# Kernel tuning notes

Hardware: AMD Instinct MI355X
Metric: run time of the kernel (lower is better)

## Reference

```python
import jax, jax.numpy as jnp
import numpy as np

B, SQ, SD, H = 64, 64, 512, 128


def setup_inputs() -> dict:
    key = jax.random.key(0)
    k1, k2, k3, k4, k5 = jax.random.split(key, 5)
    q = jax.random.normal(k1, (B, SQ, H), dtype=jnp.float32)
    d_pos = jax.random.normal(k2, (B, SD, H), dtype=jnp.float32)
    d_neg = jax.random.normal(k3, (B, SD, H), dtype=jnp.float32)
    mask_pos = jax.random.randint(k4, (B, SD), 0, 2, dtype=jnp.int32).at[:, 0].set(1)
    mask_neg = jax.random.randint(k5, (B, SD), 0, 2, dtype=jnp.int32).at[:, 0].set(1)
    return {"q": q, "d_pos": d_pos, "d_neg": d_neg,
            "mask_pos": mask_pos, "mask_neg": mask_neg}


def _colbert_maxsim(q, d, mask):
    # q: [a, s, h], d: [b, t, h], mask: [b, t] -> scores [a, b]
    simis = jnp.einsum('ash,bth->abst', q, d)            # [a, b, s, t]
    simis = jnp.where(mask[None, :, None, :] == 0, -jnp.inf, simis)
    return simis.max(axis=3).sum(axis=2)                 # max over t, sum over s


def reference(q, d_pos, d_neg, mask_pos, mask_neg):
    # Concatenate pos and in-batch-negative score blocks -> [B, 2B]
    distances = jnp.concatenate(
        [_colbert_maxsim(q, d_pos, mask_pos),
         _colbert_maxsim(q, d_neg, mask_neg)], axis=1)
    labels = jnp.arange(q.shape[0])
    logp = jax.nn.log_softmax(distances, axis=1)
    loss = -jnp.take_along_axis(logp, labels[:, None], axis=1).mean()
    return loss
```

## Files before the change

kernel.cpp:

```cpp
#include <hip/hip_runtime.h>
#include <hip/hip_bf16.h>
#include <math.h>
#include <stdint.h>

#define BB 64
#define SQN 64
#define SDN 512
#define HH 128

typedef __attribute__((ext_vector_type(8))) short bf16x8;
typedef __attribute__((ext_vector_type(16))) float f32x16;

__device__ __forceinline__ short f2bf(float f) {
  union { float f; unsigned u; } x; x.f = f;
  unsigned r = x.u + 0x7fffu + ((x.u >> 16) & 1u);
  return (short)(r >> 16);
}

__device__ __forceinline__ void gl_lds16(const short* g, short* l) {
  __builtin_amdgcn_global_load_lds(
      (const __attribute__((address_space(1))) unsigned int*)g,
      (__attribute__((address_space(3))) unsigned int*)l, 16, 0, 0);
}

__global__ __launch_bounds__(256)
void convert_all(const float* __restrict__ q, const float* __restrict__ dp,
                 const float* __restrict__ dn,
                 const int* __restrict__ mp, const int* __restrict__ mn,
                 short* __restrict__ oq, short* __restrict__ od,
                 int* __restrict__ nchunks, int* __restrict__ nvalid,
                 int* __restrict__ counter) {
  const int D_BLOCKS = (2 * BB * SDN) / 8;
  if (blockIdx.x < D_BLOCKS) {
    const int bs = blockIdx.x >> 6;
    const int j0 = (blockIdx.x & 63) * 8;
    const int side = bs >> 6, b = bs & 63;
    const int* mask = (side ? mn : mp) + b * SDN;

    __shared__ int s_perm[8];
    __shared__ int s_pad32;

    if (threadIdx.x < 64) {
      const int ln = threadIdx.x;
      int mreg[8];
      #pragma unroll
      for (int it = 0; it < 8; ++it) mreg[it] = mask[it * 64 + ln];
      int run = 0;
      #pragma unroll
      for (int it = 0; it < 8; ++it) {
        unsigned long long bal = __ballot(mreg[it] != 0);
        int pos = run + __popcll(bal & ((1ull << ln) - 1ull));
        if (mreg[it]) {
          unsigned rel = (unsigned)(pos - j0);
          if (rel < 8u) s_perm[rel] = it * 64 + ln;
        }
        run += (int)__popcll(bal);
      }
      if (ln < 8 && j0 + ln >= run) s_perm[ln] = -1;
      if (ln == 0) {
        s_pad32 = (run + 31) & ~31;
        if (j0 == 0) {
          nchunks[bs] = ((run + 127) & ~127) >> 7;
          nvalid[bs]  = run;
        }
      }
    }
    __syncthreads();

    const int j = j0 + (threadIdx.x >> 5);
    if (j >= s_pad32) return;
    const int l32 = threadIdx.x & 31;
    const int src_t = s_perm[threadIdx.x >> 5];
    const float* srcmat = side ? dn : dp;
    float4 v = make_float4(0.f, 0.f, 0.f, 0.f);
    if (src_t >= 0)
      v = ((const float4*)(srcmat + ((size_t)b * SDN + src_t) * HH))[l32];
    short4 o; o.x = f2bf(v.x); o.y = f2bf(v.y); o.z = f2bf(v.z); o.w = f2bf(v.w);
    *(short4*)&od[((size_t)bs * SDN + j) * HH + l32 * 4] = o;
  } else {
    if (blockIdx.x == D_BLOCKS && threadIdx.x == 0) *counter = 0;
    int i = (blockIdx.x - D_BLOCKS) * 256 + threadIdx.x;
    float4 v = ((const float4*)q)[i];
    short4 o; o.x = f2bf(v.x); o.y = f2bf(v.y); o.z = f2bf(v.z); o.w = f2bf(v.w);
    *(short4*)&oq[i * 4] = o;
  }
}

#define ITS_OF(bi_, tc_) \
  (((tc_) == nchv[bi_] - 1) ? (((nvv[bi_] - ((tc_) << 7) + 31) >> 5) << 1) : 8)

__global__ __launch_bounds__(256, 2)
void maxsim_kernel(const short* __restrict__ qb,
                   const short* __restrict__ dc,
                   const int* __restrict__ nchunks,
                   const int* __restrict__ nvalid,
                   float* __restrict__ scores,
                   int* __restrict__ counter,
                   float* __restrict__ out) {
  const int lid  = blockIdx.x + 16 * blockIdx.y;
  const int xcd  = lid & 7;
  const int slot = lid >> 3;
  const int aslc = slot & 15;
  const int bs0  = (xcd + 8 * (slot >> 4)) * 4;

  __shared__ __align__(16) short d_lds[2][128 * 128];

  const int tid = threadIdx.x;
  const int ln  = tid & 63;
  const int w   = tid >> 6;
  const int l31 = ln & 31;
  const int kh  = ln >> 5;
  const int a   = aslc * 4 + w;

  int nchv[4], nvv[4];
  #pragma unroll
  for (int i = 0; i < 4; ++i) {
    nchv[i] = nchunks[bs0 + i];
    nvv[i]  = nvalid[bs0 + i];
  }

  bf16x8 qfrag[2][8];
  #pragma unroll
  for (int half = 0; half < 2; ++half) {
    const short* qrow = qb + ((size_t)a * SQN + half * 32 + l31) * HH + kh * 8;
    #pragma unroll
    for (int kc = 0; kc < 8; ++kc)
      qfrag[half][kc] = *(const bf16x8*)(qrow + kc * 16);
  }

  float rmaxh[2] = {0.f, 0.f};

  int cur_its = ITS_OF(0, 0);

  {
    const short* dsrc = dc + (size_t)bs0 * SDN * HH;
    #pragma unroll
    for (int it = 0; it < 8; ++it) {
      if (it < cur_its) {
        int f = it * 256 + tid;
        int row = f >> 4;
        int c = (f & 15) ^ (row & 15);
        gl_lds16(&dsrc[row * HH + c * 8], &d_lds[0][(it * 256 + w * 64) * 8]);
      }
    }
  }
  __syncthreads();

  int bi = 0, tc = 0, buf = 0;
  for (;;) {
    int nbi = bi, ntc = tc + 1;
    if (ntc == nchv[bi]) { ntc = 0; nbi = bi + 1; }
    const bool hn = (nbi < 4);
    const int nxt_its = hn ? ITS_OF(nbi, ntc) : 0;

    if (hn) {
      const short* dsrc = dc + ((size_t)(bs0 + nbi) * SDN + ntc * 128) * HH;
      short* dst = &d_lds[buf ^ 1][0];
      #pragma unroll
      for (int it = 0; it < 8; ++it) {
        if (it < nxt_its) {
          int f = it * 256 + tid;
          int row = f >> 4;
          int c = (f & 15) ^ (row & 15);
          gl_lds16(&dsrc[row * HH + c * 8], &dst[(it * 256 + w * 64) * 8]);
        }
      }
    }

    const int ntt = cur_its >> 1;
    const short* bufp = &d_lds[buf][0];
    #pragma unroll
    for (int tt = 0; tt < 4; ++tt) {
      if (tt < ntt) {
        int trow = tt * 32 + l31;
        int tm = trow & 15;
        const short* bbase = &bufp[trow * HH];
        f32x16 acc0 = {0,0,0,0,0,0,0,0,0,0,0,0,0,0,0,0};
        f32x16 acc1 = {0,0,0,0,0,0,0,0,0,0,0,0,0,0,0,0};
        #pragma unroll
        for (int kc = 0; kc < 8; ++kc) {
          int c = (kc * 2 + kh) ^ tm;
          bf16x8 dfrag = *(const bf16x8*)&bbase[c * 8];
          acc0 = __builtin_amdgcn_mfma_f32_32x32x16_bf16(dfrag, qfrag[0][kc], acc0, 0, 0, 0);
          acc1 = __builtin_amdgcn_mfma_f32_32x32x16_bf16(dfrag, qfrag[1][kc], acc1, 0, 0, 0);
        }
        float m0 = acc0[0], m1 = acc1[0];
        #pragma unroll
        for (int r = 1; r < 16; ++r) {
          m0 = fmaxf(m0, acc0[r]);
          m1 = fmaxf(m1, acc1[r]);
        }
        rmaxh[0] = fmaxf(rmaxh[0], m0);
        rmaxh[1] = fmaxf(rmaxh[1], m1);
      }
    }

    if (ntc == 0) {
      float v0 = fmaxf(rmaxh[0], __shfl_xor(rmaxh[0], 32));
      float v1 = fmaxf(rmaxh[1], __shfl_xor(rmaxh[1], 32));
      float s = v0 + v1;
      s += __shfl_xor(s, 1);  s += __shfl_xor(s, 2);  s += __shfl_xor(s, 4);
      s += __shfl_xor(s, 8);  s += __shfl_xor(s, 16);
      if (ln == 0)
        __hip_atomic_store(&scores[(size_t)a * (2 * BB) + bs0 + bi], s,
                           __ATOMIC_RELAXED, __HIP_MEMORY_SCOPE_AGENT);
      rmaxh[0] = 0.f; rmaxh[1] = 0.f;
    }

    __syncthreads();
    if (!hn) break;
    bi = nbi; tc = ntc; buf ^= 1; cur_its = nxt_its;
  }

  asm volatile("s_waitcnt vmcnt(0)" ::: "memory");
  __shared__ int s_ticket;
  if (tid == 0)
    s_ticket = __hip_atomic_fetch_add(counter, 1,
                                      __ATOMIC_RELAXED, __HIP_MEMORY_SCOPE_AGENT);
  __syncthreads();
  if (s_ticket != 511) return;

  __shared__ float part[16];
  #pragma unroll
  for (int q8 = 0; q8 < 4; ++q8) {
    int vp = w * 4 + q8;
    float acc = 0.f;
    #pragma unroll
    for (int i = 0; i < 4; ++i) {
      int r = vp * 4 + i;
      float v0 = __hip_atomic_load(&scores[r * 128 + ln],
                                   __ATOMIC_RELAXED, __HIP_MEMORY_SCOPE_AGENT);
      float v1 = __hip_atomic_load(&scores[r * 128 + 64 + ln],
                                   __ATOMIC_RELAXED, __HIP_MEMORY_SCOPE_AGENT);
      float mx = fmaxf(v0, v1);
      #pragma unroll
      for (int off = 32; off >= 1; off >>= 1) mx = fmaxf(mx, __shfl_xor(mx, off));
      float e = __expf(v0 - mx) + __expf(v1 - mx);
      #pragma unroll
      for (int off = 32; off >= 1; off >>= 1) e += __shfl_xor(e, off);
      float lse = mx + __logf(e);
      float diag = __shfl(v0, r);
      acc += lse - diag;
    }
    if (ln == 0) part[vp] = acc;
  }
  __syncthreads();
  if (w == 0) {
    float v = (ln < 16) ? part[ln] : 0.f;
    #pragma unroll
    for (int off = 8; off >= 1; off >>= 1) v += __shfl_xor(v, off);
    if (ln == 0) out[0] = v * (1.0f / 64.0f);
  }
}

extern "C" void kernel_launch(void* const* d_in, const int* in_sizes, int n_in,
                              void* d_out, int out_size, void* d_ws, size_t ws_size,
                              hipStream_t stream) {
  const float* q        = (const float*)d_in[0];
  const float* d_pos    = (const float*)d_in[1];
  const float* d_neg    = (const float*)d_in[2];
  const int*   mask_pos = (const int*)d_in[3];
  const int*   mask_neg = (const int*)d_in[4];

  short* q_bf = (short*)d_ws;
  short* d_c  = q_bf + (size_t)BB * SQN * HH;
  int*   nchunks = (int*)(d_c + (size_t)2 * BB * SDN * HH);
  int*   nvalid  = nchunks + 128;
  float* scores  = (float*)(nvalid + 128);
  int*   counter = (int*)(scores + 64 * 128);

  const int D_BLOCKS = (2 * BB * SDN) / 8;
  const int Q_BLOCKS = (BB * SQN * HH / 4) / 256;
  convert_all<<<D_BLOCKS + Q_BLOCKS, 256, 0, stream>>>(
      q, d_pos, d_neg, mask_pos, mask_neg, q_bf, d_c, nchunks, nvalid, counter);

  dim3 grid(16 , 32 );
  maxsim_kernel<<<grid, 256, 0, stream>>>(q_bf, d_c, nchunks, nvalid, scores,
                                          counter, (float*)d_out);
}
```

Baseline: 126.8 us.

## Split query halves across two waves with 512-thread blocks

Blocks grow from 256 to 512 threads, with two waves per query row: each handles one 32-row half of the query tokens, holding one accumulator instead of two. The half-sums are combined through shared memory with an extra block barrier at each document boundary. D tile loads are spread over twice as many threads. The aim is more waves in flight and lower register pressure per wave, at the cost of extra barriers and possibly fewer resident blocks given the 64KB LDS per block.

```diff
diff --git a/kernel.cpp b/kernel.cpp
--- a/kernel.cpp
+++ b/kernel.cpp
@@ -87,9 +87,9 @@
 }
 
 #define ITS_OF(bi_, tc_) \
-  (((tc_) == nchv[bi_] - 1) ? (((nvv[bi_] - ((tc_) << 7) + 31) >> 5) << 1) : 8)
-
-__global__ __launch_bounds__(256, 2)
+  (((tc_) == nchv[bi_] - 1) ? ((nvv[bi_] - ((tc_) << 7) + 31) >> 5) : 4)
+
+__global__ __launch_bounds__(512, 4)
 void maxsim_kernel(const short* __restrict__ qb,
                    const short* __restrict__ dc,
                    const int* __restrict__ nchunks,
@@ -104,13 +104,18 @@
   const int bs0  = (xcd + 8 * (slot >> 4)) * 4;
 
   __shared__ __align__(16) short d_lds[2][128 * 128];
-
-  const int tid = threadIdx.x;
-  const int ln  = tid & 63;
-  const int w   = tid >> 6;
-  const int l31 = ln & 31;
-  const int kh  = ln >> 5;
-  const int a   = aslc * 4 + w;
+  __shared__ float s_fin[4 * 32];
+  __shared__ int s_ticket;
+  __shared__ float part[16];
+
+  const int tid  = threadIdx.x;
+  const int ln   = tid & 63;
+  const int w    = tid >> 6;
+  const int l31  = ln & 31;
+  const int kh   = ln >> 5;
+  const int aw   = w >> 1;
+  const int half = w & 1;
+  const int a    = aslc * 4 + aw;
 
   int nchv[4], nvv[4];
   #pragma unroll
@@ -119,28 +124,27 @@
     nvv[i]  = nvalid[bs0 + i];
   }
 
-  bf16x8 qfrag[2][8];
-  #pragma unroll
-  for (int half = 0; half < 2; ++half) {
+  bf16x8 qfrag[8];
+  {
     const short* qrow = qb + ((size_t)a * SQN + half * 32 + l31) * HH + kh * 8;
     #pragma unroll
     for (int kc = 0; kc < 8; ++kc)
-      qfrag[half][kc] = *(const bf16x8*)(qrow + kc * 16);
-  }
-
-  float rmaxh[2] = {0.f, 0.f};
+      qfrag[kc] = *(const bf16x8*)(qrow + kc * 16);
+  }
+
+  float rmax = 0.f;
 
   int cur_its = ITS_OF(0, 0);
 
   {
     const short* dsrc = dc + (size_t)bs0 * SDN * HH;
     #pragma unroll
-    for (int it = 0; it < 8; ++it) {
+    for (int it = 0; it < 4; ++it) {
       if (it < cur_its) {
-        int f = it * 256 + tid;
+        int f = it * 512 + tid;
         int row = f >> 4;
         int c = (f & 15) ^ (row & 15);
-        gl_lds16(&dsrc[row * HH + c * 8], &d_lds[0][(it * 256 + w * 64) * 8]);
+        gl_lds16(&dsrc[row * HH + c * 8], &d_lds[0][(it * 512 + w * 64) * 8]);
       }
     }
   }
@@ -157,17 +161,17 @@
       const short* dsrc = dc + ((size_t)(bs0 + nbi) * SDN + ntc * 128) * HH;
       short* dst = &d_lds[buf ^ 1][0];
       #pragma unroll
-      for (int it = 0; it < 8; ++it) {
+      for (int it = 0; it < 4; ++it) {
         if (it < nxt_its) {
-          int f = it * 256 + tid;
+          int f = it * 512 + tid;
           int row = f >> 4;
           int c = (f & 15) ^ (row & 15);
-          gl_lds16(&dsrc[row * HH + c * 8], &dst[(it * 256 + w * 64) * 8]);
-        }
-      }
-    }
-
-    const int ntt = cur_its >> 1;
+          gl_lds16(&dsrc[row * HH + c * 8], &dst[(it * 512 + w * 64) * 8]);
+        }
+      }
+    }
+
+    const int ntt = cur_its;
     const short* bufp = &d_lds[buf][0];
     #pragma unroll
     for (int tt = 0; tt < 4; ++tt) {
@@ -175,36 +179,33 @@
         int trow = tt * 32 + l31;
         int tm = trow & 15;
         const short* bbase = &bufp[trow * HH];
-        f32x16 acc0 = {0,0,0,0,0,0,0,0,0,0,0,0,0,0,0,0};
-        f32x16 acc1 = {0,0,0,0,0,0,0,0,0,0,0,0,0,0,0,0};
+        f32x16 acc = {0,0,0,0,0,0,0,0,0,0,0,0,0,0,0,0};
         #pragma unroll
         for (int kc = 0; kc < 8; ++kc) {
           int c = (kc * 2 + kh) ^ tm;
           bf16x8 dfrag = *(const bf16x8*)&bbase[c * 8];
-          acc0 = __builtin_amdgcn_mfma_f32_32x32x16_bf16(dfrag, qfrag[0][kc], acc0, 0, 0, 0);
-          acc1 = __builtin_amdgcn_mfma_f32_32x32x16_bf16(dfrag, qfrag[1][kc], acc1, 0, 0, 0);
-        }
-        float m0 = acc0[0], m1 = acc1[0];
-        #pragma unroll
-        for (int r = 1; r < 16; ++r) {
-          m0 = fmaxf(m0, acc0[r]);
-          m1 = fmaxf(m1, acc1[r]);
-        }
-        rmaxh[0] = fmaxf(rmaxh[0], m0);
-        rmaxh[1] = fmaxf(rmaxh[1], m1);
+          acc = __builtin_amdgcn_mfma_f32_32x32x16_bf16(dfrag, qfrag[kc], acc, 0, 0, 0);
+        }
+        float m0 = acc[0];
+        #pragma unroll
+        for (int r = 1; r < 16; ++r) m0 = fmaxf(m0, acc[r]);
+        rmax = fmaxf(rmax, m0);
       }
     }
 
     if (ntc == 0) {
-      float v0 = fmaxf(rmaxh[0], __shfl_xor(rmaxh[0], 32));
-      float v1 = fmaxf(rmaxh[1], __shfl_xor(rmaxh[1], 32));
-      float s = v0 + v1;
-      s += __shfl_xor(s, 1);  s += __shfl_xor(s, 2);  s += __shfl_xor(s, 4);
-      s += __shfl_xor(s, 8);  s += __shfl_xor(s, 16);
-      if (ln == 0)
-        __hip_atomic_store(&scores[(size_t)a * (2 * BB) + bs0 + bi], s,
-                           __ATOMIC_RELAXED, __HIP_MEMORY_SCOPE_AGENT);
-      rmaxh[0] = 0.f; rmaxh[1] = 0.f;
+      float v = fmaxf(rmax, __shfl_xor(rmax, 32));
+      if (half && kh == 0) s_fin[aw * 32 + l31] = v;
+      __syncthreads();
+      if (!half) {
+        float s = v + s_fin[aw * 32 + l31];
+        s += __shfl_xor(s, 1);  s += __shfl_xor(s, 2);  s += __shfl_xor(s, 4);
+        s += __shfl_xor(s, 8);  s += __shfl_xor(s, 16);
+        if (ln == 0)
+          __hip_atomic_store(&scores[(size_t)a * (2 * BB) + bs0 + bi], s,
+                             __ATOMIC_RELAXED, __HIP_MEMORY_SCOPE_AGENT);
+      }
+      rmax = 0.f;
     }
 
     __syncthreads();
@@ -213,36 +214,36 @@
   }
 
   asm volatile("s_waitcnt vmcnt(0)" ::: "memory");
-  __shared__ int s_ticket;
   if (tid == 0)
     s_ticket = __hip_atomic_fetch_add(counter, 1,
                                       __ATOMIC_RELAXED, __HIP_MEMORY_SCOPE_AGENT);
   __syncthreads();
   if (s_ticket != 511) return;
 
-  __shared__ float part[16];
-  #pragma unroll
-  for (int q8 = 0; q8 < 4; ++q8) {
-    int vp = w * 4 + q8;
-    float acc = 0.f;
-    #pragma unroll
-    for (int i = 0; i < 4; ++i) {
-      int r = vp * 4 + i;
-      float v0 = __hip_atomic_load(&scores[r * 128 + ln],
-                                   __ATOMIC_RELAXED, __HIP_MEMORY_SCOPE_AGENT);
-      float v1 = __hip_atomic_load(&scores[r * 128 + 64 + ln],
-                                   __ATOMIC_RELAXED, __HIP_MEMORY_SCOPE_AGENT);
-      float mx = fmaxf(v0, v1);
-      #pragma unroll
-      for (int off = 32; off >= 1; off >>= 1) mx = fmaxf(mx, __shfl_xor(mx, off));
-      float e = __expf(v0 - mx) + __expf(v1 - mx);
-      #pragma unroll
-      for (int off = 32; off >= 1; off >>= 1) e += __shfl_xor(e, off);
-      float lse = mx + __logf(e);
-      float diag = __shfl(v0, r);
-      acc += lse - diag;
-    }
-    if (ln == 0) part[vp] = acc;
+  if (w < 4) {
+    #pragma unroll
+    for (int q8 = 0; q8 < 4; ++q8) {
+      int vp = w * 4 + q8;
+      float acc = 0.f;
+      #pragma unroll
+      for (int i = 0; i < 4; ++i) {
+        int r = vp * 4 + i;
+        float v0 = __hip_atomic_load(&scores[r * 128 + ln],
+                                     __ATOMIC_RELAXED, __HIP_MEMORY_SCOPE_AGENT);
+        float v1 = __hip_atomic_load(&scores[r * 128 + 64 + ln],
+                                     __ATOMIC_RELAXED, __HIP_MEMORY_SCOPE_AGENT);
+        float mx = fmaxf(v0, v1);
+        #pragma unroll
+        for (int off = 32; off >= 1; off >>= 1) mx = fmaxf(mx, __shfl_xor(mx, off));
+        float e = __expf(v0 - mx) + __expf(v1 - mx);
+        #pragma unroll
+        for (int off = 32; off >= 1; off >>= 1) e += __shfl_xor(e, off);
+        float lse = mx + __logf(e);
+        float diag = __shfl(v0, r);
+        acc += lse - diag;
+      }
+      if (ln == 0) part[vp] = acc;
+    }
   }
   __syncthreads();
   if (w == 0) {
@@ -275,6 +276,6 @@
       q, d_pos, d_neg, mask_pos, mask_neg, q_bf, d_c, nchunks, nvalid, counter);
 
   dim3 grid(16 , 32 );
-  maxsim_kernel<<<grid, 256, 0, stream>>>(q_bf, d_c, nchunks, nvalid, scores,
+  maxsim_kernel<<<grid, 512, 0, stream>>>(q_bf, d_c, nchunks, nvalid, scores,
                                           counter, (float*)d_out);
 }
```

After: 127.9 us. No clear change (+0.9%).

## Split doc chunks across wave pairs with 4-slot LDS ring prefetch

Applied to the files above, without the earlier changes.

The block grows to 512 threads, and each pair of waves now shares one query, with each wave taking half of a 64-row doc chunk. LDS turns into a 4-slot ring of 64-row tiles staged two ahead, with the wait on vmcnt(4) plus a raw barrier. Per-doc results are merged across the wave pair through shared memory and written out once per block at the end. This is meant to raise the number of waves in flight and deepen the load pipeline. In exchange it adds an extra syncthreads on each doc finish and relies on vmcnt counting being exact, and the final iterations stage dummy loads.

```diff
diff --git a/kernel.cpp b/kernel.cpp
--- a/kernel.cpp
+++ b/kernel.cpp
@@ -86,10 +86,7 @@
   }
 }
 
-#define ITS_OF(bi_, tc_) \
-  (((tc_) == nchv[bi_] - 1) ? (((nvv[bi_] - ((tc_) << 7) + 31) >> 5) << 1) : 8)
-
-__global__ __launch_bounds__(256, 2)
+__global__ __launch_bounds__(512, 4)
 void maxsim_kernel(const short* __restrict__ qb,
                    const short* __restrict__ dc,
                    const int* __restrict__ nchunks,
@@ -99,24 +96,30 @@
                    float* __restrict__ out) {
   const int lid  = blockIdx.x + 16 * blockIdx.y;
   const int xcd  = lid & 7;
-  const int slot = lid >> 3;
-  const int aslc = slot & 15;
-  const int bs0  = (xcd + 8 * (slot >> 4)) * 4;
-
-  __shared__ __align__(16) short d_lds[2][128 * 128];
+  const int slot0= lid >> 3;
+  const int aslc = slot0 & 15;
+  const int bs0  = (xcd + 8 * (slot0 >> 4)) * 4;
+
+  __shared__ __align__(16) short d_lds[4][64 * 128];
+  __shared__ float s_fin[4 * 64];
+  __shared__ float s_out[16];
+  __shared__ int s_ticket;
+  __shared__ float part[16];
 
   const int tid = threadIdx.x;
   const int ln  = tid & 63;
   const int w   = tid >> 6;
   const int l31 = ln & 31;
   const int kh  = ln >> 5;
-  const int a   = aslc * 4 + w;
-
-  int nchv[4], nvv[4];
+  const int aw  = w >> 1;
+  const int th  = w & 1;
+  const int a   = aslc * 4 + aw;
+
+  int nch[4], nvv[4];
   #pragma unroll
   for (int i = 0; i < 4; ++i) {
-    nchv[i] = nchunks[bs0 + i];
-    nvv[i]  = nvalid[bs0 + i];
+    nvv[i] = nvalid[bs0 + i];
+    nch[i] = (nvv[i] + 63) >> 6;
   }
 
   bf16x8 qfrag[2][8];
@@ -130,119 +133,126 @@
 
   float rmaxh[2] = {0.f, 0.f};
 
-  int cur_its = ITS_OF(0, 0);
-
-  {
-    const short* dsrc = dc + (size_t)bs0 * SDN * HH;
-    #pragma unroll
-    for (int it = 0; it < 8; ++it) {
-      if (it < cur_its) {
-        int f = it * 256 + tid;
-        int row = f >> 4;
-        int c = (f & 15) ^ (row & 15);
-        gl_lds16(&dsrc[row * HH + c * 8], &d_lds[0][(it * 256 + w * 64) * 8]);
-      }
-    }
-  }
-  __syncthreads();
-
-  int bi = 0, tc = 0, buf = 0;
+  auto STAGE = [&](int pbi, int ptc, int sl) {
+    const short* dsrc = dc + ((size_t)(bs0 + pbi) * SDN + ptc * 64) * HH;
+    short* dst = &d_lds[sl][0];
+    #pragma unroll
+    for (int it = 0; it < 2; ++it) {
+      int f = it * 512 + tid;
+      int row = f >> 4;
+      int c = (f & 15) ^ (row & 15);
+      gl_lds16(&dsrc[row * HH + c * 8], &dst[(it * 512 + w * 64) * 8]);
+    }
+  };
+
+  int pbi = 0, ptc = 0;
+  STAGE(pbi, ptc, 0);
+  if (++ptc == nch[pbi]) { ptc = 0; ++pbi; }
+  STAGE(pbi, ptc, 1);
+  if (++ptc == nch[pbi]) { ptc = 0; ++pbi; }
+
+  int cbi = 0, ctc = 0, sl = 0;
   for (;;) {
-    int nbi = bi, ntc = tc + 1;
-    if (ntc == nchv[bi]) { ntc = 0; nbi = bi + 1; }
-    const bool hn = (nbi < 4);
-    const int nxt_its = hn ? ITS_OF(nbi, ntc) : 0;
-
-    if (hn) {
-      const short* dsrc = dc + ((size_t)(bs0 + nbi) * SDN + ntc * 128) * HH;
-      short* dst = &d_lds[buf ^ 1][0];
-      #pragma unroll
-      for (int it = 0; it < 8; ++it) {
-        if (it < nxt_its) {
-          int f = it * 256 + tid;
-          int row = f >> 4;
-          int c = (f & 15) ^ (row & 15);
-          gl_lds16(&dsrc[row * HH + c * 8], &dst[(it * 256 + w * 64) * 8]);
-        }
-      }
-    }
-
-    const int ntt = cur_its >> 1;
-    const short* bufp = &d_lds[buf][0];
-    #pragma unroll
-    for (int tt = 0; tt < 4; ++tt) {
-      if (tt < ntt) {
-        int trow = tt * 32 + l31;
-        int tm = trow & 15;
-        const short* bbase = &bufp[trow * HH];
-        f32x16 acc0 = {0,0,0,0,0,0,0,0,0,0,0,0,0,0,0,0};
-        f32x16 acc1 = {0,0,0,0,0,0,0,0,0,0,0,0,0,0,0,0};
-        #pragma unroll
-        for (int kc = 0; kc < 8; ++kc) {
-          int c = (kc * 2 + kh) ^ tm;
-          bf16x8 dfrag = *(const bf16x8*)&bbase[c * 8];
-          acc0 = __builtin_amdgcn_mfma_f32_32x32x16_bf16(dfrag, qfrag[0][kc], acc0, 0, 0, 0);
-          acc1 = __builtin_amdgcn_mfma_f32_32x32x16_bf16(dfrag, qfrag[1][kc], acc1, 0, 0, 0);
-        }
-        float m0 = acc0[0], m1 = acc1[0];
-        #pragma unroll
-        for (int r = 1; r < 16; ++r) {
-          m0 = fmaxf(m0, acc0[r]);
-          m1 = fmaxf(m1, acc1[r]);
-        }
-        rmaxh[0] = fmaxf(rmaxh[0], m0);
-        rmaxh[1] = fmaxf(rmaxh[1], m1);
-      }
-    }
-
-    if (ntc == 0) {
+    {
+      int qbi2 = (pbi < 4) ? pbi : 0;
+      int qtc2 = (pbi < 4) ? ptc : 0;
+      STAGE(qbi2, qtc2, (sl + 2) & 3);
+      if (pbi < 4) { if (++ptc == nch[pbi]) { ptc = 0; ++pbi; } }
+    }
+
+    asm volatile("s_waitcnt vmcnt(4)" ::: "memory");
+    __builtin_amdgcn_s_barrier();
+
+    const int ntt = (ctc == nch[cbi] - 1)
+                        ? ((nvv[cbi] - (ctc << 6) + 31) >> 5)
+                        : 2;
+    if (th < ntt) {
+      const short* bufp = &d_lds[sl][0];
+      int trow = th * 32 + l31;
+      int tm = trow & 15;
+      const short* bbase = &bufp[trow * HH];
+      f32x16 acc0 = {0,0,0,0,0,0,0,0,0,0,0,0,0,0,0,0};
+      f32x16 acc1 = {0,0,0,0,0,0,0,0,0,0,0,0,0,0,0,0};
+      #pragma unroll
+      for (int kc = 0; kc < 8; ++kc) {
+        int c = (kc * 2 + kh) ^ tm;
+        bf16x8 dfrag = *(const bf16x8*)&bbase[c * 8];
+        acc0 = __builtin_amdgcn_mfma_f32_32x32x16_bf16(dfrag, qfrag[0][kc], acc0, 0, 0, 0);
+        acc1 = __builtin_amdgcn_mfma_f32_32x32x16_bf16(dfrag, qfrag[1][kc], acc1, 0, 0, 0);
+      }
+      float m0 = acc0[0], m1 = acc1[0];
+      #pragma unroll
+      for (int r = 1; r < 16; ++r) {
+        m0 = fmaxf(m0, acc0[r]);
+        m1 = fmaxf(m1, acc1[r]);
+      }
+      rmaxh[0] = fmaxf(rmaxh[0], m0);
+      rmaxh[1] = fmaxf(rmaxh[1], m1);
+    }
+
+    const int obi = cbi;
+    const bool fin = (++ctc == nch[cbi]);
+    if (fin) {
+      ctc = 0; ++cbi;
       float v0 = fmaxf(rmaxh[0], __shfl_xor(rmaxh[0], 32));
       float v1 = fmaxf(rmaxh[1], __shfl_xor(rmaxh[1], 32));
-      float s = v0 + v1;
-      s += __shfl_xor(s, 1);  s += __shfl_xor(s, 2);  s += __shfl_xor(s, 4);
-      s += __shfl_xor(s, 8);  s += __shfl_xor(s, 16);
-      if (ln == 0)
-        __hip_atomic_store(&scores[(size_t)a * (2 * BB) + bs0 + bi], s,
-                           __ATOMIC_RELAXED, __HIP_MEMORY_SCOPE_AGENT);
+      if (th && kh == 0) {
+        s_fin[aw * 64 + l31]      = v0;
+        s_fin[aw * 64 + 32 + l31] = v1;
+      }
+      __syncthreads();
+      if (!th) {
+        v0 = fmaxf(v0, s_fin[aw * 64 + l31]);
+        v1 = fmaxf(v1, s_fin[aw * 64 + 32 + l31]);
+        float s = v0 + v1;
+        s += __shfl_xor(s, 1);  s += __shfl_xor(s, 2);  s += __shfl_xor(s, 4);
+        s += __shfl_xor(s, 8);  s += __shfl_xor(s, 16);
+        if (ln == 0) s_out[aw * 4 + obi] = s;
+      }
       rmaxh[0] = 0.f; rmaxh[1] = 0.f;
     }
 
-    __syncthreads();
-    if (!hn) break;
-    bi = nbi; tc = ntc; buf ^= 1; cur_its = nxt_its;
-  }
-
+    if (cbi == 4) break;
+    sl = (sl + 1) & 3;
+  }
+
+  __syncthreads();
+  if (w == 0 && ln < 16) {
+    int ai = ln >> 2, bi = ln & 3;
+    __hip_atomic_store(&scores[(size_t)(aslc * 4 + ai) * (2 * BB) + bs0 + bi],
+                       s_out[ln], __ATOMIC_RELAXED, __HIP_MEMORY_SCOPE_AGENT);
+  }
   asm volatile("s_waitcnt vmcnt(0)" ::: "memory");
-  __shared__ int s_ticket;
   if (tid == 0)
     s_ticket = __hip_atomic_fetch_add(counter, 1,
                                       __ATOMIC_RELAXED, __HIP_MEMORY_SCOPE_AGENT);
   __syncthreads();
   if (s_ticket != 511) return;
 
-  __shared__ float part[16];
-  #pragma unroll
-  for (int q8 = 0; q8 < 4; ++q8) {
-    int vp = w * 4 + q8;
-    float acc = 0.f;
-    #pragma unroll
-    for (int i = 0; i < 4; ++i) {
-      int r = vp * 4 + i;
-      float v0 = __hip_atomic_load(&scores[r * 128 + ln],
-                                   __ATOMIC_RELAXED, __HIP_MEMORY_SCOPE_AGENT);
-      float v1 = __hip_atomic_load(&scores[r * 128 + 64 + ln],
-                                   __ATOMIC_RELAXED, __HIP_MEMORY_SCOPE_AGENT);
-      float mx = fmaxf(v0, v1);
-      #pragma unroll
-      for (int off = 32; off >= 1; off >>= 1) mx = fmaxf(mx, __shfl_xor(mx, off));
-      float e = __expf(v0 - mx) + __expf(v1 - mx);
-      #pragma unroll
-      for (int off = 32; off >= 1; off >>= 1) e += __shfl_xor(e, off);
-      float lse = mx + __logf(e);
-      float diag = __shfl(v0, r);
-      acc += lse - diag;
-    }
-    if (ln == 0) part[vp] = acc;
+  if (w < 4) {
+    #pragma unroll
+    for (int q8 = 0; q8 < 4; ++q8) {
+      int vp = w * 4 + q8;
+      float acc = 0.f;
+      #pragma unroll
+      for (int i = 0; i < 4; ++i) {
+        int r = vp * 4 + i;
+        float v0 = __hip_atomic_load(&scores[r * 128 + ln],
+                                     __ATOMIC_RELAXED, __HIP_MEMORY_SCOPE_AGENT);
+        float v1 = __hip_atomic_load(&scores[r * 128 + 64 + ln],
+                                     __ATOMIC_RELAXED, __HIP_MEMORY_SCOPE_AGENT);
+        float mx = fmaxf(v0, v1);
+        #pragma unroll
+        for (int off = 32; off >= 1; off >>= 1) mx = fmaxf(mx, __shfl_xor(mx, off));
+        float e = __expf(v0 - mx) + __expf(v1 - mx);
+        #pragma unroll
+        for (int off = 32; off >= 1; off >>= 1) e += __shfl_xor(e, off);
+        float lse = mx + __logf(e);
+        float diag = __shfl(v0, r);
+        acc += lse - diag;
+      }
+      if (ln == 0) part[vp] = acc;
+    }
   }
   __syncthreads();
   if (w == 0) {
@@ -275,6 +285,6 @@
       q, d_pos, d_neg, mask_pos, mask_neg, q_bf, d_c, nchunks, nvalid, counter);
 
   dim3 grid(16 , 32 );
-  maxsim_kernel<<<grid, 256, 0, stream>>>(q_bf, d_c, nchunks, nvalid, scores,
+  maxsim_kernel<<<grid, 512, 0, stream>>>(q_bf, d_c, nchunks, nvalid, scores,
                                           counter, (float*)d_out);
 }
```

Result: no change. 128.4 us (+1.3%).

## Read D fragments directly from global in k-chunk-major layout, drop LDS staging

Applied to the files above, without the earlier changes.

The convert kernel now writes compacted bf16 documents in a [bs][16 k-chunks][512 rows][8] layout, so each lane's MFMA operand is one contiguous 16-byte global load. The maxsim kernel drops the double-buffered LDS pipeline and loads D fragments straight from global/L2, which frees 64KB of LDS so four blocks can run per CU. The grid doubles to 1024 blocks, with two queries per block and two waves splitting the document rows, combined through a small LDS reduction. This removes LDS traffic and barrier stalls, but it relies on L2 and cache reuse across waves and adds a per-document __syncthreads.

```diff
diff --git a/kernel.cpp b/kernel.cpp
--- a/kernel.cpp
+++ b/kernel.cpp
@@ -15,12 +15,6 @@
   union { float f; unsigned u; } x; x.f = f;
   unsigned r = x.u + 0x7fffu + ((x.u >> 16) & 1u);
   return (short)(r >> 16);
-}
-
-__device__ __forceinline__ void gl_lds16(const short* g, short* l) {
-  __builtin_amdgcn_global_load_lds(
-      (const __attribute__((address_space(1))) unsigned int*)g,
-      (__attribute__((address_space(3))) unsigned int*)l, 16, 0, 0);
 }
 
 __global__ __launch_bounds__(256)
@@ -28,16 +22,15 @@
                  const float* __restrict__ dn,
                  const int* __restrict__ mp, const int* __restrict__ mn,
                  short* __restrict__ oq, short* __restrict__ od,
-                 int* __restrict__ nchunks, int* __restrict__ nvalid,
-                 int* __restrict__ counter) {
-  const int D_BLOCKS = (2 * BB * SDN) / 8;
+                 int* __restrict__ nvalid, int* __restrict__ counter) {
+  const int D_BLOCKS = (2 * BB * SDN) / 16;
   if (blockIdx.x < D_BLOCKS) {
-    const int bs = blockIdx.x >> 6;
-    const int j0 = (blockIdx.x & 63) * 8;
+    const int bs = blockIdx.x >> 5;
+    const int j0 = (blockIdx.x & 31) * 16;
     const int side = bs >> 6, b = bs & 63;
     const int* mask = (side ? mn : mp) + b * SDN;
 
-    __shared__ int s_perm[8];
+    __shared__ int s_perm[16];
     __shared__ int s_pad32;
 
     if (threadIdx.x < 64) {
@@ -52,31 +45,35 @@
         int pos = run + __popcll(bal & ((1ull << ln) - 1ull));
         if (mreg[it]) {
           unsigned rel = (unsigned)(pos - j0);
-          if (rel < 8u) s_perm[rel] = it * 64 + ln;
+          if (rel < 16u) s_perm[rel] = it * 64 + ln;
         }
         run += (int)__popcll(bal);
       }
-      if (ln < 8 && j0 + ln >= run) s_perm[ln] = -1;
+      if (ln < 16 && j0 + ln >= run) s_perm[ln] = -1;
       if (ln == 0) {
         s_pad32 = (run + 31) & ~31;
-        if (j0 == 0) {
-          nchunks[bs] = ((run + 127) & ~127) >> 7;
-          nvalid[bs]  = run;
-        }
+        if (j0 == 0) nvalid[bs] = run;
       }
     }
     __syncthreads();
 
-    const int j = j0 + (threadIdx.x >> 5);
+    const int jrel = threadIdx.x >> 4;
+    const int c    = threadIdx.x & 15;
+    const int j    = j0 + jrel;
     if (j >= s_pad32) return;
-    const int l32 = threadIdx.x & 31;
-    const int src_t = s_perm[threadIdx.x >> 5];
+    const int src_t = s_perm[jrel];
     const float* srcmat = side ? dn : dp;
-    float4 v = make_float4(0.f, 0.f, 0.f, 0.f);
-    if (src_t >= 0)
-      v = ((const float4*)(srcmat + ((size_t)b * SDN + src_t) * HH))[l32];
-    short4 o; o.x = f2bf(v.x); o.y = f2bf(v.y); o.z = f2bf(v.z); o.w = f2bf(v.w);
-    *(short4*)&od[((size_t)bs * SDN + j) * HH + l32 * 4] = o;
+    float4 va = make_float4(0.f, 0.f, 0.f, 0.f);
+    float4 vb = make_float4(0.f, 0.f, 0.f, 0.f);
+    if (src_t >= 0) {
+      const float4* srow = (const float4*)(srcmat + ((size_t)b * SDN + src_t) * HH);
+      va = srow[c * 2];
+      vb = srow[c * 2 + 1];
+    }
+    bf16x8 o;
+    o[0] = f2bf(va.x); o[1] = f2bf(va.y); o[2] = f2bf(va.z); o[3] = f2bf(va.w);
+    o[4] = f2bf(vb.x); o[5] = f2bf(vb.y); o[6] = f2bf(vb.z); o[7] = f2bf(vb.w);
+    *(bf16x8*)&od[(((size_t)bs * 16 + c) * 512 + j) * 8] = o;
   } else {
     if (blockIdx.x == D_BLOCKS && threadIdx.x == 0) *counter = 0;
     int i = (blockIdx.x - D_BLOCKS) * 256 + threadIdx.x;
@@ -86,38 +83,35 @@
   }
 }
 
-#define ITS_OF(bi_, tc_) \
-  (((tc_) == nchv[bi_] - 1) ? (((nvv[bi_] - ((tc_) << 7) + 31) >> 5) << 1) : 8)
-
-__global__ __launch_bounds__(256, 2)
+__global__ __launch_bounds__(256, 4)
 void maxsim_kernel(const short* __restrict__ qb,
-                   const short* __restrict__ dc,
-                   const int* __restrict__ nchunks,
+                   const short* __restrict__ dct,
                    const int* __restrict__ nvalid,
                    float* __restrict__ scores,
                    int* __restrict__ counter,
                    float* __restrict__ out) {
-  const int lid  = blockIdx.x + 16 * blockIdx.y;
-  const int xcd  = lid & 7;
-  const int slot = lid >> 3;
-  const int aslc = slot & 15;
-  const int bs0  = (xcd + 8 * (slot >> 4)) * 4;
-
-  __shared__ __align__(16) short d_lds[2][128 * 128];
+  const int lid   = blockIdx.x + 32 * blockIdx.y;
+  const int xcd   = lid & 7;
+  const int slot  = lid >> 3;
+  const int aslot = slot & 31;
+  const int bs0   = (xcd + 8 * (slot >> 5)) * 4;
+
+  __shared__ float s_fin[2 * 2 * 32];
+  __shared__ int s_ticket;
+  __shared__ float part[16];
 
   const int tid = threadIdx.x;
   const int ln  = tid & 63;
   const int w   = tid >> 6;
   const int l31 = ln & 31;
   const int kh  = ln >> 5;
-  const int a   = aslc * 4 + w;
-
-  int nchv[4], nvv[4];
+  const int aw  = w >> 1;
+  const int th  = w & 1;
+  const int a   = aslot * 2 + aw;
+
+  int nvv[4];
   #pragma unroll
-  for (int i = 0; i < 4; ++i) {
-    nchv[i] = nchunks[bs0 + i];
-    nvv[i]  = nvalid[bs0 + i];
-  }
+  for (int i = 0; i < 4; ++i) nvv[i] = nvalid[bs0 + i];
 
   bf16x8 qfrag[2][8];
   #pragma unroll
@@ -128,121 +122,88 @@
       qfrag[half][kc] = *(const bf16x8*)(qrow + kc * 16);
   }
 
-  float rmaxh[2] = {0.f, 0.f};
-
-  int cur_its = ITS_OF(0, 0);
-
-  {
-    const short* dsrc = dc + (size_t)bs0 * SDN * HH;
-    #pragma unroll
-    for (int it = 0; it < 8; ++it) {
-      if (it < cur_its) {
-        int f = it * 256 + tid;
-        int row = f >> 4;
-        int c = (f & 15) ^ (row & 15);
-        gl_lds16(&dsrc[row * HH + c * 8], &d_lds[0][(it * 256 + w * 64) * 8]);
-      }
-    }
-  }
-  __syncthreads();
-
-  int bi = 0, tc = 0, buf = 0;
-  for (;;) {
-    int nbi = bi, ntc = tc + 1;
-    if (ntc == nchv[bi]) { ntc = 0; nbi = bi + 1; }
-    const bool hn = (nbi < 4);
-    const int nxt_its = hn ? ITS_OF(nbi, ntc) : 0;
-
-    if (hn) {
-      const short* dsrc = dc + ((size_t)(bs0 + nbi) * SDN + ntc * 128) * HH;
-      short* dst = &d_lds[buf ^ 1][0];
-      #pragma unroll
-      for (int it = 0; it < 8; ++it) {
-        if (it < nxt_its) {
-          int f = it * 256 + tid;
-          int row = f >> 4;
-          int c = (f & 15) ^ (row & 15);
-          gl_lds16(&dsrc[row * HH + c * 8], &dst[(it * 256 + w * 64) * 8]);
-        }
-      }
-    }
-
-    const int ntt = cur_its >> 1;
-    const short* bufp = &d_lds[buf][0];
-    #pragma unroll
-    for (int tt = 0; tt < 4; ++tt) {
-      if (tt < ntt) {
-        int trow = tt * 32 + l31;
-        int tm = trow & 15;
-        const short* bbase = &bufp[trow * HH];
-        f32x16 acc0 = {0,0,0,0,0,0,0,0,0,0,0,0,0,0,0,0};
-        f32x16 acc1 = {0,0,0,0,0,0,0,0,0,0,0,0,0,0,0,0};
-        #pragma unroll
-        for (int kc = 0; kc < 8; ++kc) {
-          int c = (kc * 2 + kh) ^ tm;
-          bf16x8 dfrag = *(const bf16x8*)&bbase[c * 8];
-          acc0 = __builtin_amdgcn_mfma_f32_32x32x16_bf16(dfrag, qfrag[0][kc], acc0, 0, 0, 0);
-          acc1 = __builtin_amdgcn_mfma_f32_32x32x16_bf16(dfrag, qfrag[1][kc], acc1, 0, 0, 0);
-        }
-        float m0 = acc0[0], m1 = acc1[0];
-        #pragma unroll
-        for (int r = 1; r < 16; ++r) {
-          m0 = fmaxf(m0, acc0[r]);
-          m1 = fmaxf(m1, acc1[r]);
-        }
-        rmaxh[0] = fmaxf(rmaxh[0], m0);
-        rmaxh[1] = fmaxf(rmaxh[1], m1);
-      }
-    }
-
-    if (ntc == 0) {
-      float v0 = fmaxf(rmaxh[0], __shfl_xor(rmaxh[0], 32));
-      float v1 = fmaxf(rmaxh[1], __shfl_xor(rmaxh[1], 32));
+  for (int bi = 0; bi < 4; ++bi) {
+    const int nv   = nvv[bi];
+    const int nc   = (nv + 63) >> 6;
+    const int nttL = ((nv - ((nc - 1) << 6)) + 31) >> 5;
+    const int myNT = (nc - 1) + (th < nttL ? 1 : 0);
+    const short* base = dct + (size_t)(bs0 + bi) * 16 * 512 * 8;
+
+    float rmaxh0 = 0.f, rmaxh1 = 0.f;
+
+    for (int t = 0; t < myNT; ++t) {
+      const int row = t * 64 + th * 32 + l31;
+      bf16x8 dv[8];
+      #pragma unroll
+      for (int kc = 0; kc < 8; ++kc)
+        dv[kc] = *(const bf16x8*)(base + (((kc * 2 + kh) * 512) + row) * 8);
+      f32x16 acc0 = {0,0,0,0,0,0,0,0,0,0,0,0,0,0,0,0};
+      f32x16 acc1 = {0,0,0,0,0,0,0,0,0,0,0,0,0,0,0,0};
+      #pragma unroll
+      for (int kc = 0; kc < 8; ++kc) {
+        acc0 = __builtin_amdgcn_mfma_f32_32x32x16_bf16(dv[kc], qfrag[0][kc], acc0, 0, 0, 0);
+        acc1 = __builtin_amdgcn_mfma_f32_32x32x16_bf16(dv[kc], qfrag[1][kc], acc1, 0, 0, 0);
+      }
+      float m0 = acc0[0], m1 = acc1[0];
+      #pragma unroll
+      for (int r = 1; r < 16; ++r) {
+        m0 = fmaxf(m0, acc0[r]);
+        m1 = fmaxf(m1, acc1[r]);
+      }
+      rmaxh0 = fmaxf(rmaxh0, m0);
+      rmaxh1 = fmaxf(rmaxh1, m1);
+    }
+
+    float v0 = fmaxf(rmaxh0, __shfl_xor(rmaxh0, 32));
+    float v1 = fmaxf(rmaxh1, __shfl_xor(rmaxh1, 32));
+    if (th && kh == 0) {
+      s_fin[(aw * 2 + 0) * 32 + l31] = v0;
+      s_fin[(aw * 2 + 1) * 32 + l31] = v1;
+    }
+    __syncthreads();
+    if (!th) {
+      v0 = fmaxf(v0, s_fin[(aw * 2 + 0) * 32 + l31]);
+      v1 = fmaxf(v1, s_fin[(aw * 2 + 1) * 32 + l31]);
       float s = v0 + v1;
       s += __shfl_xor(s, 1);  s += __shfl_xor(s, 2);  s += __shfl_xor(s, 4);
       s += __shfl_xor(s, 8);  s += __shfl_xor(s, 16);
       if (ln == 0)
         __hip_atomic_store(&scores[(size_t)a * (2 * BB) + bs0 + bi], s,
                            __ATOMIC_RELAXED, __HIP_MEMORY_SCOPE_AGENT);
-      rmaxh[0] = 0.f; rmaxh[1] = 0.f;
-    }
-
+    }
     __syncthreads();
-    if (!hn) break;
-    bi = nbi; tc = ntc; buf ^= 1; cur_its = nxt_its;
-  }
-
-  asm volatile("s_waitcnt vmcnt(0)" ::: "memory");
-  __shared__ int s_ticket;
+  }
+
   if (tid == 0)
     s_ticket = __hip_atomic_fetch_add(counter, 1,
                                       __ATOMIC_RELAXED, __HIP_MEMORY_SCOPE_AGENT);
   __syncthreads();
-  if (s_ticket != 511) return;
-
-  __shared__ float part[16];
-  #pragma unroll
-  for (int q8 = 0; q8 < 4; ++q8) {
-    int vp = w * 4 + q8;
-    float acc = 0.f;
+  if (s_ticket != 1023) return;
+
+  if (w < 4) {
     #pragma unroll
-    for (int i = 0; i < 4; ++i) {
-      int r = vp * 4 + i;
-      float v0 = __hip_atomic_load(&scores[r * 128 + ln],
-                                   __ATOMIC_RELAXED, __HIP_MEMORY_SCOPE_AGENT);
-      float v1 = __hip_atomic_load(&scores[r * 128 + 64 + ln],
-                                   __ATOMIC_RELAXED, __HIP_MEMORY_SCOPE_AGENT);
-      float mx = fmaxf(v0, v1);
-      #pragma unroll
-      for (int off = 32; off >= 1; off >>= 1) mx = fmaxf(mx, __shfl_xor(mx, off));
-      float e = __expf(v0 - mx) + __expf(v1 - mx);
-      #pragma unroll
-      for (int off = 32; off >= 1; off >>= 1) e += __shfl_xor(e, off);
-      float lse = mx + __logf(e);
-      float diag = __shfl(v0, r);
-      acc += lse - diag;
-    }
-    if (ln == 0) part[vp] = acc;
+    for (int q8 = 0; q8 < 4; ++q8) {
+      int vp = w * 4 + q8;
+      float acc = 0.f;
+      #pragma unroll
+      for (int i = 0; i < 4; ++i) {
+        int r = vp * 4 + i;
+        float v0 = __hip_atomic_load(&scores[r * 128 + ln],
+                                     __ATOMIC_RELAXED, __HIP_MEMORY_SCOPE_AGENT);
+        float v1 = __hip_atomic_load(&scores[r * 128 + 64 + ln],
+                                     __ATOMIC_RELAXED, __HIP_MEMORY_SCOPE_AGENT);
+        float mx = fmaxf(v0, v1);
+        #pragma unroll
+        for (int off = 32; off >= 1; off >>= 1) mx = fmaxf(mx, __shfl_xor(mx, off));
+        float e = __expf(v0 - mx) + __expf(v1 - mx);
+        #pragma unroll
+        for (int off = 32; off >= 1; off >>= 1) e += __shfl_xor(e, off);
+        float lse = mx + __logf(e);
+        float diag = __shfl(v0, r);
+        acc += lse - diag;
+      }
+      if (ln == 0) part[vp] = acc;
+    }
   }
   __syncthreads();
   if (w == 0) {
@@ -263,18 +224,17 @@
   const int*   mask_neg = (const int*)d_in[4];
 
   short* q_bf = (short*)d_ws;
-  short* d_c  = q_bf + (size_t)BB * SQN * HH;
-  int*   nchunks = (int*)(d_c + (size_t)2 * BB * SDN * HH);
-  int*   nvalid  = nchunks + 128;
+  short* d_ct = q_bf + (size_t)BB * SQN * HH;
+  int*   nvalid  = (int*)(d_ct + (size_t)2 * BB * SDN * HH);
   float* scores  = (float*)(nvalid + 128);
   int*   counter = (int*)(scores + 64 * 128);
 
-  const int D_BLOCKS = (2 * BB * SDN) / 8;
+  const int D_BLOCKS = (2 * BB * SDN) / 16;
   const int Q_BLOCKS = (BB * SQN * HH / 4) / 256;
   convert_all<<<D_BLOCKS + Q_BLOCKS, 256, 0, stream>>>(
-      q, d_pos, d_neg, mask_pos, mask_neg, q_bf, d_c, nchunks, nvalid, counter);
-
-  dim3 grid(16 , 32 );
-  maxsim_kernel<<<grid, 256, 0, stream>>>(q_bf, d_c, nchunks, nvalid, scores,
+      q, d_pos, d_neg, mask_pos, mask_neg, q_bf, d_ct, nvalid, counter);
+
+  dim3 grid(32 , 32 );
+  maxsim_kernel<<<grid, 256, 0, stream>>>(q_bf, d_ct, nvalid, scores,
                                           counter, (float*)d_out);
 }
```

New measurement: 136.3 us. +7.5%, slower.
